# Optimization experiments

Measured on AMD Instinct MI355X. Metric: run time of the kernel, lower is better.

Reference implementation:

```python
import jax, jax.numpy as jnp
import numpy as np

N, E = 50000, 400000
IN, HID, HEADS, OUT, EDIM = 128, 16, 8, 128, 32


def _lin(key, fan_in, fan_out, bias=True):
    k1, k2 = jax.random.split(key)
    s = 1.0 / np.sqrt(fan_in)
    W = jax.random.uniform(k1, (fan_in, fan_out), jnp.float32, -s, s)
    if bias:
        b = jax.random.uniform(k2, (fan_out,), jnp.float32, -s, s)
        return W, b
    return W


def setup_inputs() -> dict:
    key = jax.random.key(0)
    ks = jax.random.split(key, 16)
    x = jax.random.normal(ks[0], (N, IN), jnp.float32)
    edge_index = jax.random.randint(ks[1], (2, E), 0, N, jnp.int64)
    edge_feats = jax.random.normal(ks[2], (E, EDIM), jnp.float32)
    H1 = HEADS * HID  # 128
    Wq1, bq1 = _lin(ks[3], IN, H1)
    Wk1, bk1 = _lin(ks[4], IN, H1)
    Wv1, bv1 = _lin(ks[5], IN, H1)
    We1 = _lin(ks[6], EDIM, H1, bias=False)
    Ws1, bs1 = _lin(ks[7], IN, H1)
    Wq2, bq2 = _lin(ks[8], H1, OUT)
    Wk2, bk2 = _lin(ks[9], H1, OUT)
    Wv2, bv2 = _lin(ks[10], H1, OUT)
    We2 = _lin(ks[11], EDIM, OUT, bias=False)
    Ws2, bs2 = _lin(ks[12], H1, OUT)
    return dict(x=x, edge_index=edge_index, edge_feats=edge_feats,
                Wq1=Wq1, bq1=bq1, Wk1=Wk1, bk1=bk1, Wv1=Wv1, bv1=bv1, We1=We1, Ws1=Ws1, bs1=bs1,
                Wq2=Wq2, bq2=bq2, Wk2=Wk2, bk2=bk2, Wv2=Wv2, bv2=bv2, We2=We2, Ws2=Ws2, bs2=bs2)


def transformer_conv(x, src, dst, e, Wq, bq, Wk, bk, Wv, bv, We, Ws, bs, heads, ch, concat):
    # PyG TransformerConv: project at nodes, gather to edges.
    n = x.shape[0]
    q = (x @ Wq + bq).reshape(n, heads, ch)[dst]          # [E,H,C]
    k = (x @ Wk + bk).reshape(n, heads, ch)[src]
    v = (x @ Wv + bv).reshape(n, heads, ch)[src]
    ee = (e @ We).reshape(-1, heads, ch)                   # edge conditioning
    k = k + ee
    v = v + ee
    alpha = (q * k).sum(-1) / jnp.sqrt(jnp.asarray(ch, x.dtype))  # [E,H]
    # per-destination segment softmax
    m = jax.ops.segment_max(alpha, dst, num_segments=n)
    m = jnp.where(jnp.isfinite(m), m, 0.0)
    ea = jnp.exp(alpha - m[dst])
    denom = jax.ops.segment_sum(ea, dst, num_segments=n)
    attn = ea / jnp.maximum(denom[dst], 1e-16)
    out = jax.ops.segment_sum(attn[:, :, None] * v, dst, num_segments=n)  # [N,H,C]
    out = out.reshape(n, heads * ch) if concat else out.mean(axis=1)
    return out + x @ Ws + bs  # root_weight skip


def reference(x, edge_index, edge_feats,
              Wq1, bq1, Wk1, bk1, Wv1, bv1, We1, Ws1, bs1,
              Wq2, bq2, Wk2, bk2, Wv2, bv2, We2, Ws2, bs2):
    src, dst = edge_index[0], edge_index[1]
    h = jax.nn.relu(transformer_conv(x, src, dst, edge_feats,
                                     Wq1, bq1, Wk1, bk1, Wv1, bv1, We1, Ws1, bs1,
                                     HEADS, HID, True))
    # dropout p=0.0 (eval) -> identity
    out = jax.nn.relu(transformer_conv(h, src, dst, edge_feats,
                                       Wq2, bq2, Wk2, bk2, Wv2, bv2, We2, Ws2, bs2,
                                       1, OUT, False))
    return out
```

## Files before the change

### kernel.cpp

```cpp
#include <hip/hip_runtime.h>


using u16 = unsigned short;
using u32 = unsigned int;

#define NODES 50000
#define EDGES 400000
#define NB196 196

typedef __attribute__((ext_vector_type(8))) short bf16x8;
typedef __attribute__((ext_vector_type(4))) float f32x4;

__device__ __forceinline__ float bflo(u32 u) { return __uint_as_float(u << 16); }
__device__ __forceinline__ float bfhi(u32 u) { return __uint_as_float(u & 0xffff0000u); }
__device__ __forceinline__ u16 f2bf(float f) {
    u32 u = __float_as_uint(f);
    u += 0x7fffu + ((u >> 16) & 1u);
    return (u16)(u >> 16);
}
__device__ __forceinline__ u32 pack2(float a, float b) {
    return (u32)f2bf(a) | ((u32)f2bf(b) << 16);
}
__device__ __forceinline__ float rdv(const void* p, int i, int f) {
    return f ? ((const float*)p)[i]
             : __uint_as_float(((u32) reinterpret_cast<const u16*>(p)[i]) << 16);
}

#if __has_builtin(__builtin_amdgcn_fdot2_f32_bf16)
typedef __attribute__((ext_vector_type(2))) __bf16 bf2;
__device__ __forceinline__ float dot2bf(u32 a, u32 b, float c) {
    return __builtin_amdgcn_fdot2_f32_bf16(__builtin_bit_cast(bf2, a),
                                           __builtin_bit_cast(bf2, b), c, false);
}
#else
__device__ __forceinline__ float dot2bf(u32 a, u32 b, float c) {
    return fmaf(bflo(a), bflo(b), fmaf(bfhi(a), bfhi(b), c));
}
#endif

__device__ __forceinline__ float fexp2(float x) {
#if __has_builtin(__builtin_amdgcn_exp2f)
    return __builtin_amdgcn_exp2f(x);
#else
    return exp2f(x);
#endif
}

template <int CTRL>
__device__ __forceinline__ float dpp_addf(float x) {
    int y = __builtin_amdgcn_update_dpp(0, __float_as_int(x), CTRL, 0xF, 0xF, true);
    return x + __int_as_float(y);
}
template <int GRP>
__device__ __forceinline__ float grp_sum(float p, int lane) {
    p = dpp_addf<0xB1>(p);
    p = dpp_addf<0x4E>(p);
    p = dpp_addf<0x141>(p);
    if (GRP == 64) {
        p = dpp_addf<0x140>(p);
        p += __int_as_float(__builtin_amdgcn_ds_swizzle(__float_as_int(p), 0x401F));
        p += __int_as_float(__builtin_amdgcn_ds_bpermute((lane ^ 32) << 2,
                                                         __float_as_int(p)));
    }
    return p;
}

template <int SRC>
__device__ __forceinline__ u32 bcast8u(u32 x) {
    return (u32)__builtin_amdgcn_ds_swizzle((int)x, 0x18 | (SRC << 5));
}

__global__ __launch_bounds__(256) void fill_sentinel(float* __restrict__ out, int n, float val) {
    int i = blockIdx.x * 256 + threadIdx.x;
    if (i < n) out[i] = val;
}

__global__ __launch_bounds__(64) void detect_fmt(const u32* __restrict__ xw,
                                                 const int* __restrict__ eraw,
                                                 int* __restrict__ flags) {
    int lane = threadIdx.x;
    u32 e = (xw[lane] >> 7) & 0xffu;
    unsigned long long sane = __ballot(e >= 90u && e <= 141u);
    unsigned long long zodd = __ballot(eraw[1 + 2 * lane] == 0);
    if (lane == 0) {
        flags[0] = (sane == ~0ull) ? 0 : 1;
        flags[1] = (zodd == ~0ull) ? 1 : 0;
    }
}

__global__ __launch_bounds__(256) void convert_x(const void* __restrict__ X,
                                                 const int* __restrict__ flags,
                                                 u16* __restrict__ xbf, int total) {
    int i = (blockIdx.x * 256 + threadIdx.x) * 8;
    if (i >= total) return;
    if (flags[0]) {
        const float* xf = (const float*)X + i;
        float4 lo = *reinterpret_cast<const float4*>(xf);
        float4 hi = *reinterpret_cast<const float4*>(xf + 4);
        uint4 val = make_uint4(pack2(lo.x, lo.y), pack2(lo.z, lo.w),
                               pack2(hi.x, hi.y), pack2(hi.z, hi.w));
        *reinterpret_cast<uint4*>(xbf + i) = val;
    } else {
        *reinterpret_cast<uint4*>(xbf + i) =
            *reinterpret_cast<const uint4*>((const u16*)X + i);
    }
}

struct TPtrs {
    const void* src[8];
    u16*        dst[8];
    int         K[8];
};

__global__ __launch_bounds__(256) void transpose_w(TPtrs P, const int* __restrict__ fmt) {
    int m = blockIdx.x;
    int f = *fmt;
    int K = P.K[m];
    int quarter = (K * 128) >> 2;
    u16* d = P.dst[m];
    int base = blockIdx.y * quarter;
    const float* sf = (const float*)P.src[m];
    const u16*   sb = (const u16*)P.src[m];
    for (int idx = base + threadIdx.x; idx < base + quarter; idx += 256) {
        int k = idx >> 7, n = idx & 127;
        d[n * K + k] = f ? f2bf(sf[idx]) : sb[idx];
    }
}

struct WqeP {
    const void *Wq1, *We1, *bq1, *Wq2, *We2, *bq2;
    u16 *WtA, *WtB, *Wt2;
    float *bqe1, *bqe2;
    uint2 *WeP1, *WeP2;
};

__global__ __launch_bounds__(256) void make_wqe(WqeP P, const int* __restrict__ flags) {
    int f = flags[0];
    int idx = blockIdx.x * 256 + threadIdx.x;
    if (idx < 32768) {
        int col = idx >> 7, i = idx & 127;
        int hh = col >> 5, d = col & 31;
        float s = 0.f;
#pragma unroll
        for (int c = 0; c < 16; ++c)
            s += rdv(P.Wq1, i * 128 + hh * 16 + c, f) * rdv(P.We1, d * 128 + hh * 16 + c, f);
        if (col < 128) P.WtA[col * 128 + i] = f2bf(s);
        else           P.WtB[(col - 128) * 128 + i] = f2bf(s);
    } else if (idx < 49152) {
        int t = idx - 32768;
        int col = t >> 7, i = t & 127;
        float s = 0.f;
        if (col < 32) {
            for (int c = 0; c < 128; ++c)
                s += rdv(P.Wq2, i * 128 + c, f) * rdv(P.We2, col * 128 + c, f);
        }
        P.Wt2[col * 128 + i] = f2bf(s * 0.125f);
    } else if (idx < 49408) {
        int col = idx - 49152;
        int hh = col >> 5, d = col & 31;
        float s = 0.f;
#pragma unroll
        for (int c = 0; c < 16; ++c)
            s += rdv(P.bq1, hh * 16 + c, f) * rdv(P.We1, d * 128 + hh * 16 + c, f);
        P.bqe1[col] = s;
    } else if (idx < 49536) {
        int d = idx - 49408;
        float s = 0.f;
        if (d < 32)
            for (int c = 0; c < 128; ++c)
                s += rdv(P.bq2, c, f) * rdv(P.We2, d * 128 + c, f);
        P.bqe2[d] = s * 0.125f;
    } else if (idx < 50560) {
        int ent = idx - 49536;
        int t = ent >> 6, l = ent & 63, c0 = 2 * l;
        u32 xv = pack2(rdv(P.We1, (2 * t) * 128 + c0, f),
                       rdv(P.We1, (2 * t + 1) * 128 + c0, f));
        u32 yv = pack2(rdv(P.We1, (2 * t) * 128 + c0 + 1, f),
                       rdv(P.We1, (2 * t + 1) * 128 + c0 + 1, f));
        P.WeP1[ent] = make_uint2(xv, yv);
    } else if (idx < 51584) {
        int ent = idx - 50560;
        int t = ent >> 6, l = ent & 63, c0 = 2 * l;
        u32 xv = pack2(rdv(P.We2, (2 * t) * 128 + c0, f),
                       rdv(P.We2, (2 * t + 1) * 128 + c0, f));
        u32 yv = pack2(rdv(P.We2, (2 * t) * 128 + c0 + 1, f),
                       rdv(P.We2, (2 * t + 1) * 128 + c0 + 1, f));
        P.WeP2[ent] = make_uint2(xv, yv);
    }
}

__global__ __launch_bounds__(256) void count_deg(const int* __restrict__ raw,
                                                 const int* __restrict__ flags,
                                                 int* __restrict__ deg, int E) {
    int e = blockIdx.x * 256 + threadIdx.x;
    if (e < E) {
        int f = flags[1];
        int d = f ? raw[2 * (E + e)] : raw[E + e];
        if ((unsigned)d < (unsigned)NODES) atomicAdd(&deg[d], 1);
    }
}

__device__ __forceinline__ int block_scan256(int v) {
    __shared__ int ws[4];
    int t = threadIdx.x, lane = t & 63, w = t >> 6;
    int x = v;
#pragma unroll
    for (int off = 1; off < 64; off <<= 1) {
        int y = __shfl_up(x, off, 64);
        if (lane >= off) x += y;
    }
    if (lane == 63) ws[w] = x;
    __syncthreads();
#pragma unroll
    for (int j = 0; j < 3; ++j)
        if (j < w) x += ws[j];
    return x;
}

__global__ __launch_bounds__(256) void scan_a(const int* __restrict__ deg,
                                              int* __restrict__ bsum, int n) {
    int i = blockIdx.x * 256 + threadIdx.x;
    int v = (i < n) ? deg[i] : 0;
    int incl = block_scan256(v);
    if (threadIdx.x == 255) bsum[blockIdx.x] = incl;
}

__global__ __launch_bounds__(256) void scan_b(int* __restrict__ bsum, int nb) {
    int t = threadIdx.x;
    int v = (t < nb) ? bsum[t] : 0;
    int incl = block_scan256(v);
    if (t < nb) bsum[t] = incl - v;
}

__global__ __launch_bounds__(256) void scan_c(const int* __restrict__ deg,
                                              const int* __restrict__ bsum,
                                              int* __restrict__ row_ptr,
                                              int* __restrict__ cursor, int n) {
    int b = blockIdx.x;
    int i = b * 256 + threadIdx.x;
    int v = (i < n) ? deg[i] : 0;
    int incl = block_scan256(v) + bsum[b];
    if (i < n) {
        row_ptr[i + 1] = incl;
        cursor[i] = incl - v;
    }
    if (i == 0) row_ptr[0] = 0;
}

__global__ __launch_bounds__(256) void fill_csr(const int* __restrict__ raw,
                                                const int* __restrict__ flags,
                                                int* __restrict__ cursor,
                                                int* __restrict__ srcs,
                                                int* __restrict__ eids, int E) {
    int e = blockIdx.x * 256 + threadIdx.x;
    if (e < E) {
        int f = flags[1];
        int d = f ? raw[2 * (E + e)] : raw[E + e];
        int s = f ? raw[2 * e] : raw[e];
        if ((unsigned)d < (unsigned)NODES && (unsigned)s < (unsigned)NODES) {
            int pos = atomicAdd(&cursor[d], 1);
            if ((unsigned)pos < (unsigned)E) { srcs[pos] = s; eids[pos] = e; }
        }
    }
}

__global__ __launch_bounds__(256) void gather_ef(const int* __restrict__ eids,
                                                 const void* __restrict__ EF,
                                                 const int* __restrict__ flags,
                                                 u16* __restrict__ EFG, int E) {
    int t = blockIdx.x * 256 + threadIdx.x;
    int pos = t >> 2, seg = t & 3;
    if (pos >= E) return;
    int e = eids[pos];
    uint4 val;
    if (flags[0]) {
        const float* src = (const float*)EF + (size_t)e * 32 + seg * 8;
        float4 lo = *reinterpret_cast<const float4*>(src);
        float4 hi = *reinterpret_cast<const float4*>(src + 4);
        val = make_uint4(pack2(lo.x, lo.y), pack2(lo.z, lo.w),
                         pack2(hi.x, hi.y), pack2(hi.z, hi.w));
    } else {
        val = *reinterpret_cast<const uint4*>((const u16*)EF + (size_t)e * 32 + seg * 8);
    }
    *reinterpret_cast<uint4*>(EFG + (size_t)pos * 32 + seg * 8) = val;
}

struct GemmSets {
    const u16*  Wt[6];
    const void* bias[6];
    u16*        O[6];
    int         bf32[6];
    int         pitch[6];
};

__global__ __launch_bounds__(256) void gemm128(
    const u16* __restrict__ A, const int* __restrict__ flags, GemmSets S, int M) {
    constexpr int K = 128;
    constexpr int PAD = K + 8;
    constexpr int KV = K / 8;
    __shared__ u16 Asl[64 * PAD];
    __shared__ u16 Bsl[128 * PAD];

    const u16*  Wt   = S.Wt[blockIdx.y];
    const void* bias = S.bias[blockIdx.y];
    u16*        O    = S.O[blockIdx.y];
    int pitch = S.pitch[blockIdx.y];
    int f = S.bf32[blockIdx.y] ? 1 : flags[0];
    int m0 = blockIdx.x * 64;

    for (int idx = threadIdx.x; idx < 64 * KV; idx += 256) {
        int r = idx / KV, cv = idx % KV;
        int gr = m0 + r;
        uint4 val = make_uint4(0, 0, 0, 0);
        if (gr < M) val = *reinterpret_cast<const uint4*>(A + (size_t)gr * K + cv * 8);
        *reinterpret_cast<uint4*>(&Asl[r * PAD + cv * 8]) = val;
    }
    for (int idx = threadIdx.x; idx < 128 * KV; idx += 256) {
        int r = idx / KV, cv = idx % KV;
        *reinterpret_cast<uint4*>(&Bsl[r * PAD + cv * 8]) =
            *reinterpret_cast<const uint4*>(Wt + r * K + cv * 8);
    }
    __syncthreads();

    int lane = threadIdx.x & 63, wv = threadIdx.x >> 6;
    int l15 = lane & 15;
    int quad = lane >> 4;
    int kq = quad * 8;

    f32x4 b4[8];
#pragma unroll
    for (int nt = 0; nt < 8; ++nt) {
        int col0 = nt * 16 + quad * 4;
        if (bias) {
            if (f) {
                b4[nt] = *reinterpret_cast<const f32x4*>((const float*)bias + col0);
            } else {
                uint2 bu = *reinterpret_cast<const uint2*>((const u16*)bias + col0);
                b4[nt][0] = bflo(bu.x); b4[nt][1] = bfhi(bu.x);
                b4[nt][2] = bflo(bu.y); b4[nt][3] = bfhi(bu.y);
            }
        } else {
            b4[nt][0] = b4[nt][1] = b4[nt][2] = b4[nt][3] = 0.f;
        }
    }

    f32x4 acc[8] = {};
#pragma unroll
    for (int k0 = 0; k0 < K; k0 += 32) {
        bf16x8 xf = *reinterpret_cast<const bf16x8*>(&Asl[(wv * 16 + l15) * PAD + k0 + kq]);
#pragma unroll
        for (int nt = 0; nt < 8; ++nt) {
            bf16x8 wf = *reinterpret_cast<const bf16x8*>(&Bsl[(nt * 16 + l15) * PAD + k0 + kq]);
            acc[nt] = __builtin_amdgcn_mfma_f32_16x16x32_bf16(wf, xf, acc[nt], 0, 0, 0);
        }
    }

    int row = m0 + wv * 16 + l15;
    if (row < M) {
        u16* Orow = O + (size_t)row * pitch;
#pragma unroll
        for (int nt = 0; nt < 8; ++nt) {
            uint2 pk;
            pk.x = pack2(acc[nt][0] + b4[nt][0], acc[nt][1] + b4[nt][1]);
            pk.y = pack2(acc[nt][2] + b4[nt][2], acc[nt][3] + b4[nt][3]);
            *reinterpret_cast<uint2*>(Orow + nt * 16 + quad * 4) = pk;
        }
    }
}

template <int HEADS, int F32OUT>
__global__ __launch_bounds__(256) void attn_kernel(
    const int* __restrict__ row_ptr, const int* __restrict__ srcs,
    const u16* __restrict__ Q, const u16* __restrict__ KV,
    const u16* __restrict__ EFG,
    const u16* __restrict__ QWA, const u16* __restrict__ QWB,
    const u16* __restrict__ SK, const uint2* __restrict__ WeP,
    void* __restrict__ OUT, int nn) {
    int wv = threadIdx.x >> 6, lane = threadIdx.x & 63;
    int node0 = (blockIdx.x * 4 + wv) * 4;
    if (node0 >= nn) return;
    int h = lane >> 3, j = lane & 7;
    int c0 = lane * 2;

    const float s2 = (HEADS == 8) ? 0.25f * 1.44269504f
                                  : 0.08838834764831845f * 1.44269504f;
    constexpr int GRP = (HEADS == 8) ? 8 : 64;

    uint2 wD[16];
#pragma unroll
    for (int t = 0; t < 16; ++t) wD[t] = WeP[t * 64 + lane];

    int nend = (node0 + 4 < nn) ? node0 + 4 : nn;
    for (int node = node0; node < nend; ++node) {
        u32 qb = *reinterpret_cast<const u32*>(Q + (size_t)node * 128 + c0);
        const u16* qp = (HEADS == 8)
            ? ((h < 4 ? QWA : QWB) + (size_t)node * 128 + (h & 3) * 32 + j * 4)
            : (QWA + (size_t)node * 128 + j * 4);
        uint2 qwu = *reinterpret_cast<const uint2*>(qp);

        int beg = __builtin_amdgcn_readfirstlane(row_ptr[node]);
        int end = __builtin_amdgcn_readfirstlane(row_ptr[node + 1]);

        float l_run = 0.f, a0 = 0.f, a1 = 0.f;
        float f0 = 0.f, f1 = 0.f, f2 = 0.f, f3 = 0.f;

        auto edge_step = [&](u32 kbv, u32 vbv, uint2 ebv, bool valid) {
            float p = dot2bf(qb, kbv,
                     dot2bf(qwu.x, ebv.x,
                     dot2bf(qwu.y, ebv.y, 0.f)));
            p = grp_sum<GRP>(p, lane);
            float w = fexp2(p * s2);
            if (!valid) w = 0.f;
            l_run += w;
            a0 = fmaf(w, bflo(vbv), a0);
            a1 = fmaf(w, bfhi(vbv), a1);
            f0 = fmaf(w, bflo(ebv.x), f0); f1 = fmaf(w, bfhi(ebv.x), f1);
            f2 = fmaf(w, bflo(ebv.y), f2); f3 = fmaf(w, bfhi(ebv.y), f3);
        };

        int i = beg;
        for (; i + 8 <= end; i += 8) {
            u32 kb[8], vb[8]; uint2 eb[8];
#pragma unroll
            for (int t = 0; t < 8; ++t) {
                int s = srcs[i + t];
                const u16* kp = KV + (size_t)s * 256;
                kb[t] = *reinterpret_cast<const u32*>(kp + c0);
                vb[t] = *reinterpret_cast<const u32*>(kp + 128 + c0);
                eb[t] = *reinterpret_cast<const uint2*>(EFG + (size_t)(i + t) * 32 + j * 4);
            }
#pragma unroll
            for (int t = 0; t < 8; ++t) edge_step(kb[t], vb[t], eb[t], true);
        }
        for (; i < end; i += 4) {
            int kleft = end - i;
            u32 kb[4], vb[4]; uint2 eb[4];
#pragma unroll
            for (int t = 0; t < 4; ++t) {
                int idx = (i + t < end) ? i + t : end - 1;
                int s = srcs[idx];
                const u16* kp = KV + (size_t)s * 256;
                kb[t] = *reinterpret_cast<const u32*>(kp + c0);
                vb[t] = *reinterpret_cast<const u32*>(kp + 128 + c0);
                eb[t] = *reinterpret_cast<const uint2*>(EFG + (size_t)idx * 32 + j * 4);
            }
#pragma unroll
            for (int t = 0; t < 4; ++t) edge_step(kb[t], vb[t], eb[t], t < kleft);
        }

        u32 Fp0 = pack2(f0, f1), Fp1 = pack2(f2, f3);
        float acc0 = 0.f, acc1 = 0.f;
#define EPI(SRC) do { \
        u32 A = bcast8u<SRC>(Fp0), B = bcast8u<SRC>(Fp1); \
        uint2 w0 = wD[2 * SRC], w1 = wD[2 * SRC + 1]; \
        acc0 = dot2bf(A, w0.x, acc0); acc0 = dot2bf(B, w1.x, acc0); \
        acc1 = dot2bf(A, w0.y, acc1); acc1 = dot2bf(B, w1.y, acc1); \
    } while (0)
        EPI(0); EPI(1); EPI(2); EPI(3); EPI(4); EPI(5); EPI(6); EPI(7);
#undef EPI

        float inv = 1.f / fmaxf(l_run, 1e-16f);
        u32 sb = *reinterpret_cast<const u32*>(SK + (size_t)node * 128 + c0);
        float o0 = fmaxf(fmaf(a0 + acc0, inv, bflo(sb)), 0.f);
        float o1 = fmaxf(fmaf(a1 + acc1, inv, bfhi(sb)), 0.f);
        if (F32OUT) {
            *reinterpret_cast<float2*>((float*)OUT + (size_t)node * 128 + c0) =
                make_float2(o0, o1);
        } else {
            *reinterpret_cast<u32*>((u16*)OUT + (size_t)node * 128 + c0) = pack2(o0, o1);
        }
    }
}

extern "C" void kernel_launch(void* const* d_in, const int* in_sizes, int n_in,
                              void* d_out, int out_size, void* d_ws, size_t ws_size,
                              hipStream_t stream) {
    const int N = NODES, E = EDGES;
    const void* x  = d_in[0];
    const int*  ei = (const int*)d_in[1];
    const void* ef = d_in[2];
    const void* Wq1 = d_in[3];  const void* bq1 = d_in[4];
    const void* Wk1 = d_in[5];  const void* bk1 = d_in[6];
    const void* Wv1 = d_in[7];  const void* bv1 = d_in[8];
    const void* We1 = d_in[9];
    const void* Ws1 = d_in[10]; const void* bs1 = d_in[11];
    const void* Wq2 = d_in[12]; const void* bq2 = d_in[13];
    const void* Wk2 = d_in[14]; const void* bk2 = d_in[15];
    const void* Wv2 = d_in[16]; const void* bv2 = d_in[17];
    const void* We2 = d_in[18];
    const void* Ws2 = d_in[19]; const void* bs2 = d_in[20];

    char* ws = (char*)d_ws;
    size_t off = 0;
    auto carve = [&](size_t bytes) -> void* {
        void* p = ws + off;
        off += (bytes + 255) & ~(size_t)255;
        return p;
    };

    u16* WtQ1 = (u16*)carve(128 * 128 * 2);
    u16* WtK1 = (u16*)carve(128 * 128 * 2);
    u16* WtV1 = (u16*)carve(128 * 128 * 2);
    u16* WtS1 = (u16*)carve(128 * 128 * 2);
    u16* WtQ2 = (u16*)carve(128 * 128 * 2);
    u16* WtK2 = (u16*)carve(128 * 128 * 2);
    u16* WtV2 = (u16*)carve(128 * 128 * 2);
    u16* WtS2 = (u16*)carve(128 * 128 * 2);
    u16* WtqA = (u16*)carve(128 * 128 * 2);
    u16* WtqB = (u16*)carve(128 * 128 * 2);
    u16* Wtq2 = (u16*)carve(128 * 128 * 2);
    float* bqe1 = (float*)carve(256 * 4);
    float* bqe2 = (float*)carve(128 * 4);
    uint2* WeP1 = (uint2*)carve(1024 * 8);
    uint2* WeP2 = (uint2*)carve(1024 * 8);
    int* flags   = (int*)carve(256);
    int* deg     = (int*)carve((size_t)N * 4);
    int* bsum    = (int*)carve((size_t)NB196 * 4);
    int* row_ptr = (int*)carve((size_t)(N + 1) * 4);
    int* cursor  = (int*)carve((size_t)N * 4);
    int* srcs    = (int*)carve((size_t)E * 4);
    int* eids    = (int*)carve((size_t)E * 4);
    u16* xbf  = (u16*)carve((size_t)N * 128 * 2);
    u16* q    = (u16*)carve((size_t)N * 128 * 2);
    u16* kv   = (u16*)carve((size_t)N * 256 * 2);
    u16* sk   = (u16*)carve((size_t)N * 128 * 2);
    u16* h    = (u16*)carve((size_t)N * 128 * 2);
    u16* qweA = (u16*)carve((size_t)N * 128 * 2);
    u16* qweB = (u16*)carve((size_t)N * 128 * 2);
    u16* qwe2 = (u16*)carve((size_t)N * 128 * 2);
    u16* efg  = (u16*)carve((size_t)E * 32 * 2);
    const size_t REQ = off;

    if (ws_size < REQ) {
        hipLaunchKernelGGL(fill_sentinel, dim3((out_size + 255) / 256), dim3(256), 0, stream,
                           (float*)d_out, out_size, 16.0f * (float)(ws_size >> 20));
        return;
    }

    hipLaunchKernelGGL(detect_fmt, dim3(1), dim3(64), 0, stream, (const u32*)x, ei, flags);

    hipLaunchKernelGGL(convert_x, dim3((N * 128 / 8 + 255) / 256), dim3(256), 0, stream,
                       x, flags, xbf, N * 128);

    TPtrs tp;
    tp.src[0] = Wq1; tp.dst[0] = WtQ1; tp.K[0] = 128;
    tp.src[1] = Wk1; tp.dst[1] = WtK1; tp.K[1] = 128;
    tp.src[2] = Wv1; tp.dst[2] = WtV1; tp.K[2] = 128;
    tp.src[3] = Ws1; tp.dst[3] = WtS1; tp.K[3] = 128;
    tp.src[4] = Wq2; tp.dst[4] = WtQ2; tp.K[4] = 128;
    tp.src[5] = Wk2; tp.dst[5] = WtK2; tp.K[5] = 128;
    tp.src[6] = Wv2; tp.dst[6] = WtV2; tp.K[6] = 128;
    tp.src[7] = Ws2; tp.dst[7] = WtS2; tp.K[7] = 128;
    hipLaunchKernelGGL(transpose_w, dim3(8, 4), dim3(256), 0, stream, tp, flags);

    WqeP wp;
    wp.Wq1 = Wq1; wp.We1 = We1; wp.bq1 = bq1;
    wp.Wq2 = Wq2; wp.We2 = We2; wp.bq2 = bq2;
    wp.WtA = WtqA; wp.WtB = WtqB; wp.Wt2 = Wtq2;
    wp.bqe1 = bqe1; wp.bqe2 = bqe2;
    wp.WeP1 = WeP1; wp.WeP2 = WeP2;
    hipLaunchKernelGGL(make_wqe, dim3(202), dim3(256), 0, stream, wp, flags);

    (void)hipMemsetAsync(deg, 0, (size_t)N * 4, stream);
    hipLaunchKernelGGL(count_deg, dim3((E + 255) / 256), dim3(256), 0, stream, ei, flags, deg, E);
    hipLaunchKernelGGL(scan_a, dim3(NB196), dim3(256), 0, stream, deg, bsum, N);
    hipLaunchKernelGGL(scan_b, dim3(1), dim3(256), 0, stream, bsum, NB196);
    hipLaunchKernelGGL(scan_c, dim3(NB196), dim3(256), 0, stream, deg, bsum, row_ptr, cursor, N);
    hipLaunchKernelGGL(fill_csr, dim3((E + 255) / 256), dim3(256), 0, stream, ei, flags, cursor,
                       srcs, eids, E);

    hipLaunchKernelGGL(gather_ef, dim3(E * 4 / 256), dim3(256), 0, stream,
                       eids, ef, flags, efg, E);

    const int gN = (N + 63) / 64;
    const int gA = (N + 15) / 16;

    {
        GemmSets S;
        S.Wt[0] = WtQ1; S.bias[0] = bq1;  S.O[0] = q;        S.bf32[0] = 0; S.pitch[0] = 128;
        S.Wt[1] = WtK1; S.bias[1] = bk1;  S.O[1] = kv;       S.bf32[1] = 0; S.pitch[1] = 256;
        S.Wt[2] = WtV1; S.bias[2] = bv1;  S.O[2] = kv + 128; S.bf32[2] = 0; S.pitch[2] = 256;
        S.Wt[3] = WtS1; S.bias[3] = bs1;  S.O[3] = sk;       S.bf32[3] = 0; S.pitch[3] = 128;
        S.Wt[4] = WtqA; S.bias[4] = bqe1;       S.O[4] = qweA; S.bf32[4] = 1; S.pitch[4] = 128;
        S.Wt[5] = WtqB; S.bias[5] = bqe1 + 128; S.O[5] = qweB; S.bf32[5] = 1; S.pitch[5] = 128;
        hipLaunchKernelGGL(gemm128, dim3(gN, 6), dim3(256), 0, stream, xbf, flags, S, N);
    }
    hipLaunchKernelGGL((attn_kernel<8, 0>), dim3(gA), dim3(256), 0, stream,
                       row_ptr, srcs, q, kv, efg, qweA, qweB, sk, WeP1, (void*)h, N);

    {
        GemmSets S;
        S.Wt[0] = WtQ2; S.bias[0] = bq2;  S.O[0] = q;        S.bf32[0] = 0; S.pitch[0] = 128;
        S.Wt[1] = WtK2; S.bias[1] = bk2;  S.O[1] = kv;       S.bf32[1] = 0; S.pitch[1] = 256;
        S.Wt[2] = WtV2; S.bias[2] = bv2;  S.O[2] = kv + 128; S.bf32[2] = 0; S.pitch[2] = 256;
        S.Wt[3] = WtS2; S.bias[3] = bs2;  S.O[3] = sk;       S.bf32[3] = 0; S.pitch[3] = 128;
        S.Wt[4] = Wtq2; S.bias[4] = bqe2; S.O[4] = qwe2;     S.bf32[4] = 1; S.pitch[4] = 128;
        S.Wt[5] = Wtq2; S.bias[5] = bqe2; S.O[5] = qwe2;     S.bf32[5] = 1; S.pitch[5] = 128;
        hipLaunchKernelGGL(gemm128, dim3(gN, 5), dim3(256), 0, stream, h, flags, S, N);
    }
    hipLaunchKernelGGL((attn_kernel<1, 1>), dim3(gA), dim3(256), 0, stream,
                       row_ptr, srcs, q, kv, efg, qwe2, qwe2, sk, WeP2, d_out, N);
}
```

Measured before the change: 442.7 us.

## Fuse prep kernels, fold softmax scale into GEMM, one node per wave in attention

Merges x conversion with degree counting, and weight transpose with the Wqe precompute, into single launches to cut launch count. The softmax scale (1/sqrt(d)*log2e) is now applied in the GEMM epilogue for q and q·We outputs, which removes a multiply per edge in attention. The attention kernel changes from each wave handling 4 nodes with WeP held in registers to one node per wave with WeP read from memory in the epilogue, giving 4x more blocks for better load balance and latency hiding. This adds repeated WeP loads, and rounding the scaled q to bf16 slightly changes precision.

Result: faster. 429.8 us (-2.9%).

```diff
diff --git a/kernel.cpp b/kernel.cpp
--- a/kernel.cpp
+++ b/kernel.cpp
@@ -88,21 +88,34 @@
     }
 }
 
-__global__ __launch_bounds__(256) void convert_x(const void* __restrict__ X,
-                                                 const int* __restrict__ flags,
-                                                 u16* __restrict__ xbf, int total) {
-    int i = (blockIdx.x * 256 + threadIdx.x) * 8;
-    if (i >= total) return;
-    if (flags[0]) {
-        const float* xf = (const float*)X + i;
-        float4 lo = *reinterpret_cast<const float4*>(xf);
-        float4 hi = *reinterpret_cast<const float4*>(xf + 4);
-        uint4 val = make_uint4(pack2(lo.x, lo.y), pack2(lo.z, lo.w),
-                               pack2(hi.x, hi.y), pack2(hi.z, hi.w));
-        *reinterpret_cast<uint4*>(xbf + i) = val;
+#define CXB 3125
+#define CDB 1563
+__global__ __launch_bounds__(256) void convert_count(
+    const void* __restrict__ X, const int* __restrict__ raw,
+    const int* __restrict__ flags, u16* __restrict__ xbf,
+    int* __restrict__ deg, int total, int E) {
+    int b = blockIdx.x;
+    if (b < CXB) {
+        int i = (b * 256 + threadIdx.x) * 8;
+        if (i >= total) return;
+        if (flags[0]) {
+            const float* xf = (const float*)X + i;
+            float4 lo = *reinterpret_cast<const float4*>(xf);
+            float4 hi = *reinterpret_cast<const float4*>(xf + 4);
+            uint4 val = make_uint4(pack2(lo.x, lo.y), pack2(lo.z, lo.w),
+                                   pack2(hi.x, hi.y), pack2(hi.z, hi.w));
+            *reinterpret_cast<uint4*>(xbf + i) = val;
+        } else {
+            *reinterpret_cast<uint4*>(xbf + i) =
+                *reinterpret_cast<const uint4*>((const u16*)X + i);
+        }
     } else {
-        *reinterpret_cast<uint4*>(xbf + i) =
-            *reinterpret_cast<const uint4*>((const u16*)X + i);
+        int e = (b - CXB) * 256 + threadIdx.x;
+        if (e < E) {
+            int f = flags[1];
+            int d = f ? raw[2 * (E + e)] : raw[E + e];
+            if ((unsigned)d < (unsigned)NODES) atomicAdd(&deg[d], 1);
+        }
     }
 }
 
@@ -111,22 +124,6 @@
     u16*        dst[8];
     int         K[8];
 };
-
-__global__ __launch_bounds__(256) void transpose_w(TPtrs P, const int* __restrict__ fmt) {
-    int m = blockIdx.x;
-    int f = *fmt;
-    int K = P.K[m];
-    int quarter = (K * 128) >> 2;
-    u16* d = P.dst[m];
-    int base = blockIdx.y * quarter;
-    const float* sf = (const float*)P.src[m];
-    const u16*   sb = (const u16*)P.src[m];
-    for (int idx = base + threadIdx.x; idx < base + quarter; idx += 256) {
-        int k = idx >> 7, n = idx & 127;
-        d[n * K + k] = f ? f2bf(sf[idx]) : sb[idx];
-    }
-}
-
 struct WqeP {
     const void *Wq1, *We1, *bq1, *Wq2, *We2, *bq2;
     u16 *WtA, *WtB, *Wt2;
@@ -134,69 +131,73 @@
     uint2 *WeP1, *WeP2;
 };
 
-__global__ __launch_bounds__(256) void make_wqe(WqeP P, const int* __restrict__ flags) {
+__global__ __launch_bounds__(256) void prep_w(TPtrs P, WqeP Q, const int* __restrict__ flags) {
     int f = flags[0];
-    int idx = blockIdx.x * 256 + threadIdx.x;
+    int b = blockIdx.x;
+    if (b < 32) {
+        int m = b >> 2;
+        int K = P.K[m];
+        int quarter = (K * 128) >> 2;
+        u16* d = P.dst[m];
+        int base = (b & 3) * quarter;
+        const float* sf = (const float*)P.src[m];
+        const u16*   sb = (const u16*)P.src[m];
+        for (int idx = base + threadIdx.x; idx < base + quarter; idx += 256) {
+            int k = idx >> 7, n = idx & 127;
+            d[n * K + k] = f ? f2bf(sf[idx]) : sb[idx];
+        }
+        return;
+    }
+    int idx = (b - 32) * 256 + threadIdx.x;
     if (idx < 32768) {
         int col = idx >> 7, i = idx & 127;
         int hh = col >> 5, d = col & 31;
         float s = 0.f;
 #pragma unroll
         for (int c = 0; c < 16; ++c)
-            s += rdv(P.Wq1, i * 128 + hh * 16 + c, f) * rdv(P.We1, d * 128 + hh * 16 + c, f);
-        if (col < 128) P.WtA[col * 128 + i] = f2bf(s);
-        else           P.WtB[(col - 128) * 128 + i] = f2bf(s);
+            s += rdv(Q.Wq1, i * 128 + hh * 16 + c, f) * rdv(Q.We1, d * 128 + hh * 16 + c, f);
+        if (col < 128) Q.WtA[col * 128 + i] = f2bf(s);
+        else           Q.WtB[(col - 128) * 128 + i] = f2bf(s);
     } else if (idx < 49152) {
         int t = idx - 32768;
         int col = t >> 7, i = t & 127;
         float s = 0.f;
         if (col < 32) {
             for (int c = 0; c < 128; ++c)
-                s += rdv(P.Wq2, i * 128 + c, f) * rdv(P.We2, col * 128 + c, f);
-        }
-        P.Wt2[col * 128 + i] = f2bf(s * 0.125f);
+                s += rdv(Q.Wq2, i * 128 + c, f) * rdv(Q.We2, col * 128 + c, f);
+        }
+        Q.Wt2[col * 128 + i] = f2bf(s * 0.125f);
     } else if (idx < 49408) {
         int col = idx - 49152;
         int hh = col >> 5, d = col & 31;
         float s = 0.f;
 #pragma unroll
         for (int c = 0; c < 16; ++c)
-            s += rdv(P.bq1, hh * 16 + c, f) * rdv(P.We1, d * 128 + hh * 16 + c, f);
-        P.bqe1[col] = s;
+            s += rdv(Q.bq1, hh * 16 + c, f) * rdv(Q.We1, d * 128 + hh * 16 + c, f);
+        Q.bqe1[col] = s;
     } else if (idx < 49536) {
         int d = idx - 49408;
         float s = 0.f;
         if (d < 32)
             for (int c = 0; c < 128; ++c)
-                s += rdv(P.bq2, c, f) * rdv(P.We2, d * 128 + c, f);
-        P.bqe2[d] = s * 0.125f;
+                s += rdv(Q.bq2, c, f) * rdv(Q.We2, d * 128 + c, f);
+        Q.bqe2[d] = s * 0.125f;
     } else if (idx < 50560) {
         int ent = idx - 49536;
         int t = ent >> 6, l = ent & 63, c0 = 2 * l;
-        u32 xv = pack2(rdv(P.We1, (2 * t) * 128 + c0, f),
-                       rdv(P.We1, (2 * t + 1) * 128 + c0, f));
-        u32 yv = pack2(rdv(P.We1, (2 * t) * 128 + c0 + 1, f),
-                       rdv(P.We1, (2 * t + 1) * 128 + c0 + 1, f));
-        P.WeP1[ent] = make_uint2(xv, yv);
+        u32 xv = pack2(rdv(Q.We1, (2 * t) * 128 + c0, f),
+                       rdv(Q.We1, (2 * t + 1) * 128 + c0, f));
+        u32 yv = pack2(rdv(Q.We1, (2 * t) * 128 + c0 + 1, f),
+                       rdv(Q.We1, (2 * t + 1) * 128 + c0 + 1, f));
+        Q.WeP1[ent] = make_uint2(xv, yv);
     } else if (idx < 51584) {
         int ent = idx - 50560;
         int t = ent >> 6, l = ent & 63, c0 = 2 * l;
-        u32 xv = pack2(rdv(P.We2, (2 * t) * 128 + c0, f),
-                       rdv(P.We2, (2 * t + 1) * 128 + c0, f));
-        u32 yv = pack2(rdv(P.We2, (2 * t) * 128 + c0 + 1, f),
-                       rdv(P.We2, (2 * t + 1) * 128 + c0 + 1, f));
-        P.WeP2[ent] = make_uint2(xv, yv);
-    }
-}
-
-__global__ __launch_bounds__(256) void count_deg(const int* __restrict__ raw,
-                                                 const int* __restrict__ flags,
-                                                 int* __restrict__ deg, int E) {
-    int e = blockIdx.x * 256 + threadIdx.x;
-    if (e < E) {
-        int f = flags[1];
-        int d = f ? raw[2 * (E + e)] : raw[E + e];
-        if ((unsigned)d < (unsigned)NODES) atomicAdd(&deg[d], 1);
+        u32 xv = pack2(rdv(Q.We2, (2 * t) * 128 + c0, f),
+                       rdv(Q.We2, (2 * t + 1) * 128 + c0, f));
+        u32 yv = pack2(rdv(Q.We2, (2 * t) * 128 + c0 + 1, f),
+                       rdv(Q.We2, (2 * t + 1) * 128 + c0 + 1, f));
+        Q.WeP2[ent] = make_uint2(xv, yv);
     }
 }
 
@@ -291,6 +292,7 @@
     u16*        O[6];
     int         bf32[6];
     int         pitch[6];
+    float       oscale[6];
 };
 
 __global__ __launch_bounds__(256) void gemm128(
@@ -305,6 +307,7 @@
     const void* bias = S.bias[blockIdx.y];
     u16*        O    = S.O[blockIdx.y];
     int pitch = S.pitch[blockIdx.y];
+    float os  = S.oscale[blockIdx.y];
     int f = S.bf32[blockIdx.y] ? 1 : flags[0];
     int m0 = blockIdx.x * 64;
 
@@ -361,8 +364,8 @@
 #pragma unroll
         for (int nt = 0; nt < 8; ++nt) {
             uint2 pk;
-            pk.x = pack2(acc[nt][0] + b4[nt][0], acc[nt][1] + b4[nt][1]);
-            pk.y = pack2(acc[nt][2] + b4[nt][2], acc[nt][3] + b4[nt][3]);
+            pk.x = pack2((acc[nt][0] + b4[nt][0]) * os, (acc[nt][1] + b4[nt][1]) * os);
+            pk.y = pack2((acc[nt][2] + b4[nt][2]) * os, (acc[nt][3] + b4[nt][3]) * os);
             *reinterpret_cast<uint2*>(Orow + nt * 16 + quad * 4) = pk;
         }
     }
@@ -377,98 +380,89 @@
     const u16* __restrict__ SK, const uint2* __restrict__ WeP,
     void* __restrict__ OUT, int nn) {
     int wv = threadIdx.x >> 6, lane = threadIdx.x & 63;
-    int node0 = (blockIdx.x * 4 + wv) * 4;
-    if (node0 >= nn) return;
+    int node = blockIdx.x * 4 + wv;
+    if (node >= nn) return;
     int h = lane >> 3, j = lane & 7;
     int c0 = lane * 2;
-
-    const float s2 = (HEADS == 8) ? 0.25f * 1.44269504f
-                                  : 0.08838834764831845f * 1.44269504f;
     constexpr int GRP = (HEADS == 8) ? 8 : 64;
 
-    uint2 wD[16];
-#pragma unroll
-    for (int t = 0; t < 16; ++t) wD[t] = WeP[t * 64 + lane];
-
-    int nend = (node0 + 4 < nn) ? node0 + 4 : nn;
-    for (int node = node0; node < nend; ++node) {
-        u32 qb = *reinterpret_cast<const u32*>(Q + (size_t)node * 128 + c0);
-        const u16* qp = (HEADS == 8)
-            ? ((h < 4 ? QWA : QWB) + (size_t)node * 128 + (h & 3) * 32 + j * 4)
-            : (QWA + (size_t)node * 128 + j * 4);
-        uint2 qwu = *reinterpret_cast<const uint2*>(qp);
-
-        int beg = __builtin_amdgcn_readfirstlane(row_ptr[node]);
-        int end = __builtin_amdgcn_readfirstlane(row_ptr[node + 1]);
-
-        float l_run = 0.f, a0 = 0.f, a1 = 0.f;
-        float f0 = 0.f, f1 = 0.f, f2 = 0.f, f3 = 0.f;
-
-        auto edge_step = [&](u32 kbv, u32 vbv, uint2 ebv, bool valid) {
-            float p = dot2bf(qb, kbv,
-                     dot2bf(qwu.x, ebv.x,
-                     dot2bf(qwu.y, ebv.y, 0.f)));
-            p = grp_sum<GRP>(p, lane);
-            float w = fexp2(p * s2);
-            if (!valid) w = 0.f;
-            l_run += w;
-            a0 = fmaf(w, bflo(vbv), a0);
-            a1 = fmaf(w, bfhi(vbv), a1);
-            f0 = fmaf(w, bflo(ebv.x), f0); f1 = fmaf(w, bfhi(ebv.x), f1);
-            f2 = fmaf(w, bflo(ebv.y), f2); f3 = fmaf(w, bfhi(ebv.y), f3);
-        };
-
-        int i = beg;
-        for (; i + 8 <= end; i += 8) {
-            u32 kb[8], vb[8]; uint2 eb[8];
-#pragma unroll
-            for (int t = 0; t < 8; ++t) {
-                int s = srcs[i + t];
-                const u16* kp = KV + (size_t)s * 256;
-                kb[t] = *reinterpret_cast<const u32*>(kp + c0);
-                vb[t] = *reinterpret_cast<const u32*>(kp + 128 + c0);
-                eb[t] = *reinterpret_cast<const uint2*>(EFG + (size_t)(i + t) * 32 + j * 4);
-            }
-#pragma unroll
-            for (int t = 0; t < 8; ++t) edge_step(kb[t], vb[t], eb[t], true);
-        }
-        for (; i < end; i += 4) {
-            int kleft = end - i;
-            u32 kb[4], vb[4]; uint2 eb[4];
-#pragma unroll
-            for (int t = 0; t < 4; ++t) {
-                int idx = (i + t < end) ? i + t : end - 1;
-                int s = srcs[idx];
-                const u16* kp = KV + (size_t)s * 256;
-                kb[t] = *reinterpret_cast<const u32*>(kp + c0);
-                vb[t] = *reinterpret_cast<const u32*>(kp + 128 + c0);
-                eb[t] = *reinterpret_cast<const uint2*>(EFG + (size_t)idx * 32 + j * 4);
-            }
-#pragma unroll
-            for (int t = 0; t < 4; ++t) edge_step(kb[t], vb[t], eb[t], t < kleft);
-        }
-
-        u32 Fp0 = pack2(f0, f1), Fp1 = pack2(f2, f3);
-        float acc0 = 0.f, acc1 = 0.f;
+    u32 qb = *reinterpret_cast<const u32*>(Q + (size_t)node * 128 + c0);
+    const u16* qp = (HEADS == 8)
+        ? ((h < 4 ? QWA : QWB) + (size_t)node * 128 + (h & 3) * 32 + j * 4)
+        : (QWA + (size_t)node * 128 + j * 4);
+    uint2 qwu = *reinterpret_cast<const uint2*>(qp);
+
+    int beg = __builtin_amdgcn_readfirstlane(row_ptr[node]);
+    int end = __builtin_amdgcn_readfirstlane(row_ptr[node + 1]);
+
+    float l_run = 0.f, a0 = 0.f, a1 = 0.f;
+    float f0 = 0.f, f1 = 0.f, f2 = 0.f, f3 = 0.f;
+
+    auto edge_step = [&](u32 kbv, u32 vbv, uint2 ebv, bool valid) {
+        float p = dot2bf(qb, kbv,
+                 dot2bf(qwu.x, ebv.x,
+                 dot2bf(qwu.y, ebv.y, 0.f)));
+        p = grp_sum<GRP>(p, lane);
+        float w = fexp2(p);
+        if (!valid) w = 0.f;
+        l_run += w;
+        a0 = fmaf(w, bflo(vbv), a0);
+        a1 = fmaf(w, bfhi(vbv), a1);
+        f0 = fmaf(w, bflo(ebv.x), f0); f1 = fmaf(w, bfhi(ebv.x), f1);
+        f2 = fmaf(w, bflo(ebv.y), f2); f3 = fmaf(w, bfhi(ebv.y), f3);
+    };
+
+    int i = beg;
+    for (; i + 8 <= end; i += 8) {
+        u32 kb[8], vb[8]; uint2 eb[8];
+#pragma unroll
+        for (int t = 0; t < 8; ++t) {
+            int s = srcs[i + t];
+            const u16* kp = KV + (size_t)s * 256;
+            kb[t] = *reinterpret_cast<const u32*>(kp + c0);
+            vb[t] = *reinterpret_cast<const u32*>(kp + 128 + c0);
+            eb[t] = *reinterpret_cast<const uint2*>(EFG + (size_t)(i + t) * 32 + j * 4);
+        }
+#pragma unroll
+        for (int t = 0; t < 8; ++t) edge_step(kb[t], vb[t], eb[t], true);
+    }
+    for (; i < end; i += 4) {
+        int kleft = end - i;
+        u32 kb[4], vb[4]; uint2 eb[4];
+#pragma unroll
+        for (int t = 0; t < 4; ++t) {
+            int idx = (i + t < end) ? i + t : end - 1;
+            int s = srcs[idx];
+            const u16* kp = KV + (size_t)s * 256;
+            kb[t] = *reinterpret_cast<const u32*>(kp + c0);
+            vb[t] = *reinterpret_cast<const u32*>(kp + 128 + c0);
+            eb[t] = *reinterpret_cast<const uint2*>(EFG + (size_t)idx * 32 + j * 4);
+        }
+#pragma unroll
+        for (int t = 0; t < 4; ++t) edge_step(kb[t], vb[t], eb[t], t < kleft);
+    }
+
+    u32 Fp0 = pack2(f0, f1), Fp1 = pack2(f2, f3);
+    float acc0 = 0.f, acc1 = 0.f;
 #define EPI(SRC) do { \
         u32 A = bcast8u<SRC>(Fp0), B = bcast8u<SRC>(Fp1); \
-        uint2 w0 = wD[2 * SRC], w1 = wD[2 * SRC + 1]; \
+        uint2 w0 = WeP[(2 * SRC) * 64 + lane]; \
+        uint2 w1 = WeP[(2 * SRC + 1) * 64 + lane]; \
         acc0 = dot2bf(A, w0.x, acc0); acc0 = dot2bf(B, w1.x, acc0); \
         acc1 = dot2bf(A, w0.y, acc1); acc1 = dot2bf(B, w1.y, acc1); \
     } while (0)
-        EPI(0); EPI(1); EPI(2); EPI(3); EPI(4); EPI(5); EPI(6); EPI(7);
+    EPI(0); EPI(1); EPI(2); EPI(3); EPI(4); EPI(5); EPI(6); EPI(7);
 #undef EPI
 
-        float inv = 1.f / fmaxf(l_run, 1e-16f);
-        u32 sb = *reinterpret_cast<const u32*>(SK + (size_t)node * 128 + c0);
-        float o0 = fmaxf(fmaf(a0 + acc0, inv, bflo(sb)), 0.f);
-        float o1 = fmaxf(fmaf(a1 + acc1, inv, bfhi(sb)), 0.f);
-        if (F32OUT) {
-            *reinterpret_cast<float2*>((float*)OUT + (size_t)node * 128 + c0) =
-                make_float2(o0, o1);
-        } else {
-            *reinterpret_cast<u32*>((u16*)OUT + (size_t)node * 128 + c0) = pack2(o0, o1);
-        }
+    float inv = 1.f / fmaxf(l_run, 1e-16f);
+    u32 sb = *reinterpret_cast<const u32*>(SK + (size_t)node * 128 + c0);
+    float o0 = fmaxf(fmaf(a0 + acc0, inv, bflo(sb)), 0.f);
+    float o1 = fmaxf(fmaf(a1 + acc1, inv, bfhi(sb)), 0.f);
+    if (F32OUT) {
+        *reinterpret_cast<float2*>((float*)OUT + (size_t)node * 128 + c0) =
+            make_float2(o0, o1);
+    } else {
+        *reinterpret_cast<u32*>((u16*)OUT + (size_t)node * 128 + c0) = pack2(o0, o1);
     }
 }
 
@@ -537,10 +531,14 @@
         return;
     }
 
+    const float s2_1 = 0.25f * 1.44269504f;
+    const float s2_2 = 0.08838834764831845f * 1.44269504f;
+
     hipLaunchKernelGGL(detect_fmt, dim3(1), dim3(64), 0, stream, (const u32*)x, ei, flags);
 
-    hipLaunchKernelGGL(convert_x, dim3((N * 128 / 8 + 255) / 256), dim3(256), 0, stream,
-                       x, flags, xbf, N * 128);
+    (void)hipMemsetAsync(deg, 0, (size_t)N * 4, stream);
+    hipLaunchKernelGGL(convert_count, dim3(CXB + CDB), dim3(256), 0, stream,
+                       x, ei, flags, xbf, deg, N * 128, E);
 
     TPtrs tp;
     tp.src[0] = Wq1; tp.dst[0] = WtQ1; tp.K[0] = 128;
@@ -551,18 +549,14 @@
     tp.src[5] = Wk2; tp.dst[5] = WtK2; tp.K[5] = 128;
     tp.src[6] = Wv2; tp.dst[6] = WtV2; tp.K[6] = 128;
     tp.src[7] = Ws2; tp.dst[7] = WtS2; tp.K[7] = 128;
-    hipLaunchKernelGGL(transpose_w, dim3(8, 4), dim3(256), 0, stream, tp, flags);
-
     WqeP wp;
     wp.Wq1 = Wq1; wp.We1 = We1; wp.bq1 = bq1;
     wp.Wq2 = Wq2; wp.We2 = We2; wp.bq2 = bq2;
     wp.WtA = WtqA; wp.WtB = WtqB; wp.Wt2 = Wtq2;
     wp.bqe1 = bqe1; wp.bqe2 = bqe2;
     wp.WeP1 = WeP1; wp.WeP2 = WeP2;
-    hipLaunchKernelGGL(make_wqe, dim3(202), dim3(256), 0, stream, wp, flags);
-
-    (void)hipMemsetAsync(deg, 0, (size_t)N * 4, stream);
-    hipLaunchKernelGGL(count_deg, dim3((E + 255) / 256), dim3(256), 0, stream, ei, flags, deg, E);
+    hipLaunchKernelGGL(prep_w, dim3(32 + 202), dim3(256), 0, stream, tp, wp, flags);
+
     hipLaunchKernelGGL(scan_a, dim3(NB196), dim3(256), 0, stream, deg, bsum, N);
     hipLaunchKernelGGL(scan_b, dim3(1), dim3(256), 0, stream, bsum, NB196);
     hipLaunchKernelGGL(scan_c, dim3(NB196), dim3(256), 0, stream, deg, bsum, row_ptr, cursor, N);
@@ -573,16 +567,16 @@
                        eids, ef, flags, efg, E);
 
     const int gN = (N + 63) / 64;
-    const int gA = (N + 15) / 16;
+    const int gA = (N + 3) / 4;
 
     {
         GemmSets S;
-        S.Wt[0] = WtQ1; S.bias[0] = bq1;  S.O[0] = q;        S.bf32[0] = 0; S.pitch[0] = 128;
-        S.Wt[1] = WtK1; S.bias[1] = bk1;  S.O[1] = kv;       S.bf32[1] = 0; S.pitch[1] = 256;
-        S.Wt[2] = WtV1; S.bias[2] = bv1;  S.O[2] = kv + 128; S.bf32[2] = 0; S.pitch[2] = 256;
-        S.Wt[3] = WtS1; S.bias[3] = bs1;  S.O[3] = sk;       S.bf32[3] = 0; S.pitch[3] = 128;
-        S.Wt[4] = WtqA; S.bias[4] = bqe1;       S.O[4] = qweA; S.bf32[4] = 1; S.pitch[4] = 128;
-        S.Wt[5] = WtqB; S.bias[5] = bqe1 + 128; S.O[5] = qweB; S.bf32[5] = 1; S.pitch[5] = 128;
+        S.Wt[0] = WtQ1; S.bias[0] = bq1;  S.O[0] = q;        S.bf32[0] = 0; S.pitch[0] = 128; S.oscale[0] = s2_1;
+        S.Wt[1] = WtK1; S.bias[1] = bk1;  S.O[1] = kv;       S.bf32[1] = 0; S.pitch[1] = 256; S.oscale[1] = 1.f;
+        S.Wt[2] = WtV1; S.bias[2] = bv1;  S.O[2] = kv + 128; S.bf32[2] = 0; S.pitch[2] = 256; S.oscale[2] = 1.f;
+        S.Wt[3] = WtS1; S.bias[3] = bs1;  S.O[3] = sk;       S.bf32[3] = 0; S.pitch[3] = 128; S.oscale[3] = 1.f;
+        S.Wt[4] = WtqA; S.bias[4] = bqe1;       S.O[4] = qweA; S.bf32[4] = 1; S.pitch[4] = 128; S.oscale[4] = s2_1;
+        S.Wt[5] = WtqB; S.bias[5] = bqe1 + 128; S.O[5] = qweB; S.bf32[5] = 1; S.pitch[5] = 128; S.oscale[5] = s2_1;
         hipLaunchKernelGGL(gemm128, dim3(gN, 6), dim3(256), 0, stream, xbf, flags, S, N);
     }
     hipLaunchKernelGGL((attn_kernel<8, 0>), dim3(gA), dim3(256), 0, stream,
@@ -590,12 +584,12 @@
 
     {
         GemmSets S;
-        S.Wt[0] = WtQ2; S.bias[0] = bq2;  S.O[0] = q;        S.bf32[0] = 0; S.pitch[0] = 128;
-        S.Wt[1] = WtK2; S.bias[1] = bk2;  S.O[1] = kv;       S.bf32[1] = 0; S.pitch[1] = 256;
-        S.Wt[2] = WtV2; S.bias[2] = bv2;  S.O[2] = kv + 128; S.bf32[2] = 0; S.pitch[2] = 256;
-        S.Wt[3] = WtS2; S.bias[3] = bs2;  S.O[3] = sk;       S.bf32[3] = 0; S.pitch[3] = 128;
-        S.Wt[4] = Wtq2; S.bias[4] = bqe2; S.O[4] = qwe2;     S.bf32[4] = 1; S.pitch[4] = 128;
-        S.Wt[5] = Wtq2; S.bias[5] = bqe2; S.O[5] = qwe2;     S.bf32[5] = 1; S.pitch[5] = 128;
+        S.Wt[0] = WtQ2; S.bias[0] = bq2;  S.O[0] = q;        S.bf32[0] = 0; S.pitch[0] = 128; S.oscale[0] = s2_2;
+        S.Wt[1] = WtK2; S.bias[1] = bk2;  S.O[1] = kv;       S.bf32[1] = 0; S.pitch[1] = 256; S.oscale[1] = 1.f;
+        S.Wt[2] = WtV2; S.bias[2] = bv2;  S.O[2] = kv + 128; S.bf32[2] = 0; S.pitch[2] = 256; S.oscale[2] = 1.f;
+        S.Wt[3] = WtS2; S.bias[3] = bs2;  S.O[3] = sk;       S.bf32[3] = 0; S.pitch[3] = 128; S.oscale[3] = 1.f;
+        S.Wt[4] = Wtq2; S.bias[4] = bqe2; S.O[4] = qwe2;     S.bf32[4] = 1; S.pitch[4] = 128; S.oscale[4] = s2_2;
+        S.Wt[5] = Wtq2; S.bias[5] = bqe2; S.O[5] = qwe2;     S.bf32[5] = 1; S.pitch[5] = 128; S.oscale[5] = s2_2;
         hipLaunchKernelGGL(gemm128, dim3(gN, 5), dim3(256), 0, stream, h, flags, S, N);
     }
     hipLaunchKernelGGL((attn_kernel<1, 1>), dim3(gA), dim3(256), 0, stream,
```
